# Performance work log

Hardware: AMD Instinct MI355X
Metric: run time of the kernel (lower is better)

The kernel has to match this reference:

```python
import jax, jax.numpy as jnp
import numpy as np


def _layernorm(x, g, b, eps=1e-5):
    m = x.mean(-1, keepdims=True)
    v = ((x - m) ** 2).mean(-1, keepdims=True)
    return (x - m) * jax.lax.rsqrt(v + eps) * g + b


def setup_inputs() -> dict:
    dim, B, N = 128, 1, 1024
    key = jax.random.key(0)
    ks = jax.random.split(key, 8)
    s = lambda fan_in: 1.0 / np.sqrt(fan_in)
    return {
        "x": jax.random.normal(ks[0], (B, N, dim), jnp.float32),
        # node_encoder: Linear(dim, 2dim) -> LayerNorm(2dim) -> GELU -> Linear(2dim, dim)
        "W_enc1": jax.random.normal(ks[1], (dim, 2 * dim), jnp.float32) * s(dim),
        "b_enc1": jnp.zeros((2 * dim,), jnp.float32),
        "ln_g": jnp.ones((2 * dim,), jnp.float32),
        "ln_b": jnp.zeros((2 * dim,), jnp.float32),
        "W_enc2": jax.random.normal(ks[2], (2 * dim, dim), jnp.float32) * s(2 * dim),
        "b_enc2": jnp.zeros((dim,), jnp.float32),
        # edge_predictor: Linear(2dim, dim) -> GELU -> Linear(dim, 1) -> Sigmoid
        "W_e1": jax.random.normal(ks[3], (2 * dim, dim), jnp.float32) * s(2 * dim),
        "b_e1": jnp.zeros((dim,), jnp.float32),
        "W_e2": jax.random.normal(ks[4], (dim, 1), jnp.float32) * s(dim),
        "b_e2": jnp.zeros((1,), jnp.float32),
        "threshold": jnp.full((1,), 0.5, jnp.float32),
    }


def reference(x, W_enc1, b_enc1, ln_g, ln_b, W_enc2, b_enc2,
              W_e1, b_e1, W_e2, b_e2, threshold):
    dim = x.shape[-1]
    # node encoder (exact-erf GELU, matching torch default)
    h = _layernorm(x @ W_enc1 + b_enc1, ln_g, ln_b)
    node_feats = jax.nn.gelu(h, approximate=False) @ W_enc2 + b_enc2  # [B,N,dim]

    # Edge predictor on all pairs. cat([f_i, f_j]) @ W_e1 == f_i @ W_e1[:dim] + f_j @ W_e1[dim:]
    # -> avoids materializing the [B,N,N,2*dim] concat; hidden is [B,N,N,dim].
    hi = node_feats @ W_e1[:dim]   # [B,N,dim]
    hj = node_feats @ W_e1[dim:]   # [B,N,dim]
    pair_h = jax.nn.gelu(hi[:, :, None, :] + hj[:, None, :, :] + b_e1,
                         approximate=False)            # [B,N,N,dim]
    logits = pair_h @ W_e2 + b_e2                      # [B,N,N,1]
    probs = jax.nn.sigmoid(logits)
    # F.gumbel_softmax(probs, tau=1, hard=False) over last axis of size 1:
    # softmax over a singleton axis is identically 1.0, independent of gumbel noise.
    edge_probs = jnp.ones_like(probs)
    adj_matrix = (edge_probs > threshold).astype(jnp.float32)  # [B,N,N,1]
    return adj_matrix, node_feats
```

## Files before the change

kernel.cpp:

```cpp
#include <hip/hip_runtime.h>
#include <math.h>

#define DIM 128
#define H   256
#define ROWS 8
#define NROWS 1024
#define NODE_BLOCKS (NROWS / ROWS)
#define ADJ_SIZE (NROWS * NROWS)
#define FILL_BLOCKS (ADJ_SIZE / (256 * 4))


__global__ __launch_bounds__(256) void fused_graphgen(
    const float* __restrict__ x,
    const float* __restrict__ W1, const float* __restrict__ b1,
    const float* __restrict__ lng, const float* __restrict__ lnb,
    const float* __restrict__ W2, const float* __restrict__ b2,
    const float* __restrict__ thr,
    float* __restrict__ out)
{
    const int blk = blockIdx.x;
    const int tid = threadIdx.x;

    if (blk >= NODE_BLOCKS) {
        const int fb = blk - NODE_BLOCKS;
        const float a = (1.0f > thr[0]) ? 1.0f : 0.0f;
        float4 v = make_float4(a, a, a, a);
        ((float4*)out)[fb * 256 + tid] = v;
        return;
    }

    __shared__ float xs[ROWS * DIM];
    __shared__ float hbuf[ROWS * H];
    __shared__ float mu_s[ROWS], ri_s[ROWS];

    const float4* xsrc = (const float4*)(x + (size_t)blk * ROWS * DIM);
    ((float4*)xs)[tid] = xsrc[tid];
    __syncthreads();

    float acc[ROWS];
    #pragma unroll
    for (int r = 0; r < ROWS; ++r) acc[r] = 0.0f;
    for (int k = 0; k < DIM; ++k) {
        float w = W1[k * H + tid];
        #pragma unroll
        for (int r = 0; r < ROWS; ++r) acc[r] += xs[r * DIM + k] * w;
    }
    {
        float bb = b1[tid];
        #pragma unroll
        for (int r = 0; r < ROWS; ++r) hbuf[r * H + tid] = acc[r] + bb;
    }
    __syncthreads();

    {
        int grp = tid >> 5, lane = tid & 31;
        float s = 0.0f, ss = 0.0f;
        #pragma unroll
        for (int m = 0; m < H / 32; ++m) {
            float v = hbuf[grp * H + lane + m * 32];
            s += v; ss += v * v;
        }
        #pragma unroll
        for (int off = 16; off >= 1; off >>= 1) {
            s  += __shfl_down(s,  off, 32);
            ss += __shfl_down(ss, off, 32);
        }
        if (lane == 0) {
            float mu  = s * (1.0f / H);
            float var = ss * (1.0f / H) - mu * mu;
            mu_s[grp] = mu;
            ri_s[grp] = rsqrtf(var + 1e-5f);
        }
    }
    __syncthreads();

    {
        float g_ = lng[tid], bln = lnb[tid];
        #pragma unroll
        for (int r = 0; r < ROWS; ++r) {
            float v  = hbuf[r * H + tid];
            float hn = (v - mu_s[r]) * ri_s[r] * g_ + bln;
            float ge = 0.5f * hn * (1.0f + erff(hn * 0.70710678118654752f));
            hbuf[r * H + tid] = ge;
        }
    }
    __syncthreads();

    {
        int i  = tid & 127;
        int r0 = tid >> 7;
        float o[4];
        #pragma unroll
        for (int k = 0; k < 4; ++k) o[k] = 0.0f;
        for (int j = 0; j < H; ++j) {
            float w = W2[j * DIM + i];
            #pragma unroll
            for (int k = 0; k < 4; ++k) o[k] += hbuf[(r0 + 2 * k) * H + j] * w;
        }
        float be = b2[i];
        float* nf = out + ADJ_SIZE + (size_t)blk * ROWS * DIM;
        #pragma unroll
        for (int k = 0; k < 4; ++k) {
            nf[(r0 + 2 * k) * DIM + i] = o[k] + be;
        }
    }
}

extern "C" void kernel_launch(void* const* d_in, const int* in_sizes, int n_in,
                              void* d_out, int out_size, void* d_ws, size_t ws_size,
                              hipStream_t stream) {
    const float* x    = (const float*)d_in[0];
    const float* W1   = (const float*)d_in[1];
    const float* b1   = (const float*)d_in[2];
    const float* lng  = (const float*)d_in[3];
    const float* lnb  = (const float*)d_in[4];
    const float* W2   = (const float*)d_in[5];
    const float* b2   = (const float*)d_in[6];
    const float* thr  = (const float*)d_in[11];
    float* out = (float*)d_out;

    fused_graphgen<<<NODE_BLOCKS + FILL_BLOCKS, 256, 0, stream>>>(
        x, W1, b1, lng, lnb, W2, b2, thr, out);
}
```

Measured before the change: 95.13 us.

## Halve rows per node block and split second GEMM reduction across half-blocks

Rows per block drop from 8 to 4, doubling the number of node-encoder blocks so more CUs share the work. The first GEMM reads x directly from global memory as float4 instead of staging it in shared memory. LayerNorm and GELU are fused into a single pass with one wavefront per row and a 64-lane xor reduction. The second GEMM splits the K dimension between the two 128-thread halves and combines them through shared memory, giving each thread fewer serial steps. The cost is more global reads of W1 and W2 across blocks and an extra barrier for the partial-sum reduction.

```diff
diff --git a/kernel.cpp b/kernel.cpp
--- a/kernel.cpp
+++ b/kernel.cpp
@@ -3,7 +3,7 @@
 
 #define DIM 128
 #define H   256
-#define ROWS 8
+#define ROWS 4
 #define NROWS 1024
 #define NODE_BLOCKS (NROWS / ROWS)
 #define ADJ_SIZE (NROWS * NROWS)
@@ -24,84 +24,97 @@
     if (blk >= NODE_BLOCKS) {
         const int fb = blk - NODE_BLOCKS;
         const float a = (1.0f > thr[0]) ? 1.0f : 0.0f;
-        float4 v = make_float4(a, a, a, a);
-        ((float4*)out)[fb * 256 + tid] = v;
+        ((float4*)out)[fb * 256 + tid] = make_float4(a, a, a, a);
         return;
     }
 
-    __shared__ float xs[ROWS * DIM];
     __shared__ float hbuf[ROWS * H];
-    __shared__ float mu_s[ROWS], ri_s[ROWS];
+    __shared__ float red[ROWS * DIM];
 
-    const float4* xsrc = (const float4*)(x + (size_t)blk * ROWS * DIM);
-    ((float4*)xs)[tid] = xsrc[tid];
-    __syncthreads();
+    const float* xr = x + (size_t)blk * ROWS * DIM;
 
-    float acc[ROWS];
-    #pragma unroll
-    for (int r = 0; r < ROWS; ++r) acc[r] = 0.0f;
-    for (int k = 0; k < DIM; ++k) {
-        float w = W1[k * H + tid];
-        #pragma unroll
-        for (int r = 0; r < ROWS; ++r) acc[r] += xs[r * DIM + k] * w;
+    float a0 = 0.f, a1 = 0.f, a2 = 0.f, a3 = 0.f;
+    #pragma unroll 4
+    for (int k4 = 0; k4 < DIM / 4; ++k4) {
+        const int k = k4 * 4;
+        const float4 x0 = *(const float4*)(xr + 0 * DIM + k);
+        const float4 x1 = *(const float4*)(xr + 1 * DIM + k);
+        const float4 x2 = *(const float4*)(xr + 2 * DIM + k);
+        const float4 x3 = *(const float4*)(xr + 3 * DIM + k);
+        const float w0 = W1[(k + 0) * H + tid];
+        const float w1 = W1[(k + 1) * H + tid];
+        const float w2 = W1[(k + 2) * H + tid];
+        const float w3 = W1[(k + 3) * H + tid];
+        a0 += x0.x * w0 + x0.y * w1 + x0.z * w2 + x0.w * w3;
+        a1 += x1.x * w0 + x1.y * w1 + x1.z * w2 + x1.w * w3;
+        a2 += x2.x * w0 + x2.y * w1 + x2.z * w2 + x2.w * w3;
+        a3 += x3.x * w0 + x3.y * w1 + x3.z * w2 + x3.w * w3;
     }
     {
-        float bb = b1[tid];
-        #pragma unroll
-        for (int r = 0; r < ROWS; ++r) hbuf[r * H + tid] = acc[r] + bb;
+        const float bb = b1[tid];
+        hbuf[0 * H + tid] = a0 + bb;
+        hbuf[1 * H + tid] = a1 + bb;
+        hbuf[2 * H + tid] = a2 + bb;
+        hbuf[3 * H + tid] = a3 + bb;
     }
     __syncthreads();
 
     {
-        int grp = tid >> 5, lane = tid & 31;
-        float s = 0.0f, ss = 0.0f;
+        const int w = tid >> 6, lane = tid & 63;
+        float4 v = ((float4*)hbuf)[w * (H / 4) + lane];
+        float s  = v.x + v.y + v.z + v.w;
+        float ss = v.x * v.x + v.y * v.y + v.z * v.z + v.w * v.w;
         #pragma unroll
-        for (int m = 0; m < H / 32; ++m) {
-            float v = hbuf[grp * H + lane + m * 32];
-            s += v; ss += v * v;
+        for (int m = 32; m >= 1; m >>= 1) {
+            s  += __shfl_xor(s,  m, 64);
+            ss += __shfl_xor(ss, m, 64);
         }
-        #pragma unroll
-        for (int off = 16; off >= 1; off >>= 1) {
-            s  += __shfl_down(s,  off, 32);
-            ss += __shfl_down(ss, off, 32);
-        }
-        if (lane == 0) {
-            float mu  = s * (1.0f / H);
-            float var = ss * (1.0f / H) - mu * mu;
-            mu_s[grp] = mu;
-            ri_s[grp] = rsqrtf(var + 1e-5f);
-        }
+        const float mu = s * (1.0f / H);
+        const float ri = rsqrtf(ss * (1.0f / H) - mu * mu + 1e-5f);
+        const float4 g4 = ((const float4*)lng)[lane];
+        const float4 b4 = ((const float4*)lnb)[lane];
+        float t;
+        t = (v.x - mu) * ri * g4.x + b4.x; v.x = 0.5f * t * (1.0f + erff(t * 0.70710678118654752f));
+        t = (v.y - mu) * ri * g4.y + b4.y; v.y = 0.5f * t * (1.0f + erff(t * 0.70710678118654752f));
+        t = (v.z - mu) * ri * g4.z + b4.z; v.z = 0.5f * t * (1.0f + erff(t * 0.70710678118654752f));
+        t = (v.w - mu) * ri * g4.w + b4.w; v.w = 0.5f * t * (1.0f + erff(t * 0.70710678118654752f));
+        ((float4*)hbuf)[w * (H / 4) + lane] = v;
     }
     __syncthreads();
 
     {
-        float g_ = lng[tid], bln = lnb[tid];
-        #pragma unroll
-        for (int r = 0; r < ROWS; ++r) {
-            float v  = hbuf[r * H + tid];
-            float hn = (v - mu_s[r]) * ri_s[r] * g_ + bln;
-            float ge = 0.5f * hn * (1.0f + erff(hn * 0.70710678118654752f));
-            hbuf[r * H + tid] = ge;
+        const int i = tid & 127, h = tid >> 7;
+        float o0 = 0.f, o1 = 0.f, o2 = 0.f, o3 = 0.f;
+        #pragma unroll 4
+        for (int j4 = 0; j4 < 32; ++j4) {
+            const int j = h * 128 + j4 * 4;
+            const float4 h0 = ((float4*)hbuf)[(0 * H + j) >> 2];
+            const float4 h1 = ((float4*)hbuf)[(1 * H + j) >> 2];
+            const float4 h2 = ((float4*)hbuf)[(2 * H + j) >> 2];
+            const float4 h3 = ((float4*)hbuf)[(3 * H + j) >> 2];
+            const float w0 = W2[(j + 0) * DIM + i];
+            const float w1 = W2[(j + 1) * DIM + i];
+            const float w2 = W2[(j + 2) * DIM + i];
+            const float w3 = W2[(j + 3) * DIM + i];
+            o0 += h0.x * w0 + h0.y * w1 + h0.z * w2 + h0.w * w3;
+            o1 += h1.x * w0 + h1.y * w1 + h1.z * w2 + h1.w * w3;
+            o2 += h2.x * w0 + h2.y * w1 + h2.z * w2 + h2.w * w3;
+            o3 += h3.x * w0 + h3.y * w1 + h3.z * w2 + h3.w * w3;
         }
-    }
-    __syncthreads();
-
-    {
-        int i  = tid & 127;
-        int r0 = tid >> 7;
-        float o[4];
-        #pragma unroll
-        for (int k = 0; k < 4; ++k) o[k] = 0.0f;
-        for (int j = 0; j < H; ++j) {
-            float w = W2[j * DIM + i];
-            #pragma unroll
-            for (int k = 0; k < 4; ++k) o[k] += hbuf[(r0 + 2 * k) * H + j] * w;
+        if (h == 1) {
+            red[0 * DIM + i] = o0;
+            red[1 * DIM + i] = o1;
+            red[2 * DIM + i] = o2;
+            red[3 * DIM + i] = o3;
         }
-        float be = b2[i];
-        float* nf = out + ADJ_SIZE + (size_t)blk * ROWS * DIM;
-        #pragma unroll
-        for (int k = 0; k < 4; ++k) {
-            nf[(r0 + 2 * k) * DIM + i] = o[k] + be;
+        __syncthreads();
+        if (h == 0) {
+            const float be = b2[i];
+            float* nf = out + ADJ_SIZE + (size_t)blk * ROWS * DIM;
+            nf[0 * DIM + i] = o0 + red[0 * DIM + i] + be;
+            nf[1 * DIM + i] = o1 + red[1 * DIM + i] + be;
+            nf[2 * DIM + i] = o2 + red[2 * DIM + i] + be;
+            nf[3 * DIM + i] = o3 + red[3 * DIM + i] + be;
         }
     }
 }
```

Result: faster. 84.50 us (-11.2%).
